# Kernel optimization log

Measured on AMD Instinct MI355X. Metric: run time of the kernel, lower is better.

## Reference

```python
import jax, jax.numpy as jnp
import numpy as np

D = 4096  # domain size of every variable X, Y, Z, W


def setup_inputs() -> dict:
    key = jax.random.key(0)
    ks = jax.random.split(key, 7)
    theta0 = jax.random.normal(ks[0], (D, D), dtype=jnp.float32)  # clique (X, Y)
    theta1 = jax.random.normal(ks[1], (D, D), dtype=jnp.float32)  # clique (Y, Z)
    theta2 = jax.random.normal(ks[2], (D, D), dtype=jnp.float32)  # clique (Z, W)
    ops = {f"op{i}": jax.random.randint(ks[3 + i], (2, D), 0, D, dtype=jnp.int32)
           for i in range(4)}
    return {"theta0": theta0, "theta1": theta1, "theta2": theta2, **ops}


def _remap(proc, op, dom):
    # torch: zeros(dom).index_add_(0, op[1], proc[op[0]])
    return jnp.zeros((dom,), proc.dtype).at[op[1]].add(proc[op[0]])


def reference(theta0, theta1, theta2, op0, op1, op2, op3):
    dom = theta0.shape[0]
    # m0: clique0 -> clique1 (forward): sum over X (dim 0), remap Y, broadcast over Z
    m0 = _remap(jnp.sum(theta0, axis=0), op0, dom)
    theta1 = theta1 + m0[:, None]          # reshape_dims [True, False]
    # m1: clique1 -> clique2 (forward): sum over Y (dim 0), remap Z
    m1 = _remap(jnp.sum(theta1, axis=0), op1, dom)
    theta2 = theta2 + m1[:, None]
    # m2: clique2 -> clique1 (backward): sum over W (dim 1), subtract stored fwd msg m1
    m2 = _remap(jnp.sum(theta2, axis=1) - m1, op2, dom)
    theta1 = theta1 + m2[None, :]          # reshape_dims [False, True]
    # m3: clique1 -> clique0 (backward): sum over Z (dim 1), subtract stored fwd msg m0
    m3 = _remap(jnp.sum(theta1, axis=1) - m0, op3, dom)
    theta0 = theta0 + m3[None, :]
    return (theta0, theta1, theta2)
```

## Files before the change

kernel.cpp:

```cpp
#include <hip/hip_runtime.h>

#define D 4096

typedef float fx4 __attribute__((ext_vector_type(4)));

#define CS0 0
#define CS1 D
#define RS1 (2 * D)
#define RS2 (3 * D)
#define M0O (4 * D)
#define M1O (5 * D)
#define M2O (6 * D)
#define M3O (7 * D)

__global__ void __launch_bounds__(256) reduce_kernel(
        const float* __restrict__ t0, const float* __restrict__ t1,
        float* __restrict__ ws) {
    int b = blockIdx.x;
    if (b < 512) {
        const float* A = (b < 256) ? t0 : t1;
        float* out = ws + ((b < 256) ? CS0 : CS1);
        int lb = b & 255;
        int c4 = (lb & 3) * 256 + threadIdx.x;
        int r0 = (lb >> 2) * 64;
        const fx4* A4 = (const fx4*)A;
        fx4 s = (fx4){0.f, 0.f, 0.f, 0.f};
        #pragma unroll 8
        for (int r = 0; r < 64; ++r)
            s += A4[(size_t)(r0 + r) * (D / 4) + c4];
        atomicAdd(&out[c4 * 4 + 0], s.x);
        atomicAdd(&out[c4 * 4 + 1], s.y);
        atomicAdd(&out[c4 * 4 + 2], s.z);
        atomicAdd(&out[c4 * 4 + 3], s.w);
    } else {
        int lb = b - 512;
        int wid = threadIdx.x >> 6, lane = threadIdx.x & 63;
        int row = lb * 4 + wid;
        const fx4* R = (const fx4*)(t1 + (size_t)row * D);
        float s = 0.f;
        #pragma unroll
        for (int j = 0; j < 16; ++j) {
            fx4 v = R[lane + 64 * j];
            s += (v.x + v.y) + (v.z + v.w);
        }
        #pragma unroll
        for (int o = 32; o > 0; o >>= 1) s += __shfl_down(s, o);
        if (lane == 0) ws[RS1 + row] = s;
    }
}


__device__ __forceinline__ float block_sum_1024(float v, float* red) {
    #pragma unroll
    for (int o = 32; o > 0; o >>= 1) v += __shfl_down(v, o);
    int lane = threadIdx.x & 63, wid = threadIdx.x >> 6;
    if (lane == 0) red[wid] = v;
    __syncthreads();
    if (threadIdx.x == 0) {
        float t = 0.f;
        #pragma unroll
        for (int w = 0; w < 16; ++w) t += red[w];
        red[0] = t;
    }
    __syncthreads();
    float r = red[0];
    __syncthreads();
    return r;
}

__global__ void __launch_bounds__(1024) msgsA_kernel(
        float* __restrict__ ws, const int* __restrict__ op0,
        const int* __restrict__ op1) {
    __shared__ float m0[D], m1[D];
    __shared__ float red[16];
    int tid = threadIdx.x;

    int s0[4], d0[4], s1[4], d1[4];
    #pragma unroll
    for (int k = 0; k < 4; ++k) {
        int i = tid + k * 1024;
        s0[k] = op0[i]; d0[k] = op0[D + i];
        s1[k] = op1[i]; d1[k] = op1[D + i];
    }
    float g0[4], g1[4];
    #pragma unroll
    for (int k = 0; k < 4; ++k) {
        g0[k] = ws[CS0 + s0[k]];
        g1[k] = ws[CS1 + s1[k]];
    }
    #pragma unroll
    for (int k = 0; k < 4; ++k) {
        int i = tid + k * 1024;
        m0[i] = 0.f; m1[i] = 0.f;
    }
    __syncthreads();
    #pragma unroll
    for (int k = 0; k < 4; ++k) atomicAdd(&m0[d0[k]], g0[k]);
    __syncthreads();
    float p = 0.f;
    #pragma unroll
    for (int k = 0; k < 4; ++k) p += m0[tid + k * 1024];
    float S0 = block_sum_1024(p, red);
    #pragma unroll
    for (int k = 0; k < 4; ++k) atomicAdd(&m1[d1[k]], g1[k] + S0);
    __syncthreads();
    #pragma unroll
    for (int k = 0; k < 4; ++k) {
        int i = tid + k * 1024;
        ws[M0O + i] = m0[i];
        ws[M1O + i] = m1[i];
    }
}

__global__ void __launch_bounds__(1024) msgsBC_kernel(
        float* __restrict__ ws, const int* __restrict__ op2,
        const int* __restrict__ op3) {
    __shared__ float m2[D], m3[D];
    __shared__ float red[16];
    int tid = threadIdx.x;

    int s2[4], d2[4], s3[4], d3[4];
    #pragma unroll
    for (int k = 0; k < 4; ++k) {
        int i = tid + k * 1024;
        s2[k] = op2[i]; d2[k] = op2[D + i];
        s3[k] = op3[i]; d3[k] = op3[D + i];
    }
    float g2[4], g3p[4];
    #pragma unroll
    for (int k = 0; k < 4; ++k) {
        g2[k]  = ws[RS2 + s2[k]] + 4095.0f * ws[M1O + s2[k]];
        g3p[k] = ws[RS1 + s3[k]] + 4095.0f * ws[M0O + s3[k]];
    }
    #pragma unroll
    for (int k = 0; k < 4; ++k) {
        int i = tid + k * 1024;
        m2[i] = 0.f; m3[i] = 0.f;
    }
    __syncthreads();
    #pragma unroll
    for (int k = 0; k < 4; ++k) atomicAdd(&m2[d2[k]], g2[k]);
    __syncthreads();
    float p = 0.f;
    #pragma unroll
    for (int k = 0; k < 4; ++k) p += m2[tid + k * 1024];
    float S2 = block_sum_1024(p, red);
    #pragma unroll
    for (int k = 0; k < 4; ++k) atomicAdd(&m3[d3[k]], g3p[k] + S2);
    __syncthreads();
    #pragma unroll
    for (int k = 0; k < 4; ++k) {
        int i = tid + k * 1024;
        ws[M2O + i] = m2[i];
        ws[M3O + i] = m3[i];
    }
}


__device__ __forceinline__ void row_reduce_store(float s, float* dst) {
    __shared__ float red[4];
    #pragma unroll
    for (int o = 32; o > 0; o >>= 1) s += __shfl_down(s, o);
    int lane = threadIdx.x & 63, wid = threadIdx.x >> 6;
    if (lane == 0) red[wid] = s;
    __syncthreads();
    if (threadIdx.x == 0) *dst = (red[0] + red[1]) + (red[2] + red[3]);
}

__global__ void __launch_bounds__(256) applyT2_kernel(
        const float* __restrict__ t2, float* __restrict__ ws,
        float* __restrict__ out2) {
    int row = blockIdx.x;
    size_t base = (size_t)row * D;
    const fx4* src = (const fx4*)(t2 + base);
    fx4* dst = (fx4*)(out2 + base);
    float rr = ws[M1O + row];

    fx4 v[4];
    float s = 0.f;
    #pragma unroll
    for (int k = 0; k < 4; ++k) {
        v[k] = src[threadIdx.x + 256 * k];
        s += (v[k].x + v[k].y) + (v[k].z + v[k].w);
    }
    #pragma unroll
    for (int k = 0; k < 4; ++k)
        __builtin_nontemporal_store(v[k] + rr, &dst[threadIdx.x + 256 * k]);
    row_reduce_store(s, ws + RS2 + row);
}

__global__ void __launch_bounds__(256) applyT1_kernel(
        const float* __restrict__ t1, const float* __restrict__ ws,
        float* __restrict__ out1) {
    int row = blockIdx.x;
    size_t base = (size_t)row * D;
    const fx4* src = (const fx4*)(t1 + base);
    const fx4* c4 = (const fx4*)(ws + M2O);
    fx4* dst = (fx4*)(out1 + base);
    float rr = ws[M0O + row];

    #pragma unroll
    for (int k = 0; k < 4; ++k) {
        fx4 r = src[threadIdx.x + 256 * k] + c4[threadIdx.x + 256 * k] + rr;
        __builtin_nontemporal_store(r, &dst[threadIdx.x + 256 * k]);
    }
}

__global__ void __launch_bounds__(256) applyT0_kernel(
        const float* __restrict__ t0, const float* __restrict__ ws,
        float* __restrict__ out0) {
    int row = blockIdx.x;
    size_t base = (size_t)row * D;
    const fx4* src = (const fx4*)(t0 + base);
    const fx4* c4 = (const fx4*)(ws + M3O);
    fx4* dst = (fx4*)(out0 + base);

    #pragma unroll
    for (int k = 0; k < 4; ++k) {
        fx4 r = src[threadIdx.x + 256 * k] + c4[threadIdx.x + 256 * k];
        __builtin_nontemporal_store(r, &dst[threadIdx.x + 256 * k]);
    }
}

extern "C" void kernel_launch(void* const* d_in, const int* in_sizes, int n_in,
                              void* d_out, int out_size, void* d_ws, size_t ws_size,
                              hipStream_t stream) {
    const float* t0 = (const float*)d_in[0];
    const float* t1 = (const float*)d_in[1];
    const float* t2 = (const float*)d_in[2];
    const int* op0 = (const int*)d_in[3];
    const int* op1 = (const int*)d_in[4];
    const int* op2 = (const int*)d_in[5];
    const int* op3 = (const int*)d_in[6];
    float* out = (float*)d_out;
    float* ws = (float*)d_ws;

    hipMemsetAsync(ws, 0, 2 * D * sizeof(float), stream);

    reduce_kernel<<<1536, 256, 0, stream>>>(t0, t1, ws);
    msgsA_kernel<<<1, 1024, 0, stream>>>(ws, op0, op1);
    applyT2_kernel<<<D, 256, 0, stream>>>(t2, ws, out + 2 * (size_t)D * D);
    msgsBC_kernel<<<1, 1024, 0, stream>>>(ws, op2, op3);
    applyT1_kernel<<<D, 256, 0, stream>>>(t1, ws, out + 1 * (size_t)D * D);
    applyT0_kernel<<<D, 256, 0, stream>>>(t0, ws, out + 0 * (size_t)D * D);
}
```

Before: 140.6 us.

## Fuse t1 row sums into column reduction pass and merge final apply kernels

The reduce kernel now computes t1's row sums in the same pass that accumulates its column sums, using per-row wave shuffles and a shared-memory partial array with atomics, instead of re-reading t1 in separate blocks. This removes one full 64MB read of t1. The t1 and t0 apply kernels are merged into a single launch of 2*D blocks, saving a launch and its tail. In exchange the t1 reduction blocks do a shuffle reduction per row, which adds ALU and shuffle work to a memory-bound loop, and the reduce grid drops to 512 blocks, which may leave the GPU under-occupied.

Measured after the change: 148.9 us. 1.06x slower.

```diff
diff --git a/kernel.cpp b/kernel.cpp
--- a/kernel.cpp
+++ b/kernel.cpp
@@ -16,36 +16,47 @@
 __global__ void __launch_bounds__(256) reduce_kernel(
         const float* __restrict__ t0, const float* __restrict__ t1,
         float* __restrict__ ws) {
-    int b = blockIdx.x;
-    if (b < 512) {
-        const float* A = (b < 256) ? t0 : t1;
-        float* out = ws + ((b < 256) ? CS0 : CS1);
-        int lb = b & 255;
-        int c4 = (lb & 3) * 256 + threadIdx.x;
-        int r0 = (lb >> 2) * 64;
-        const fx4* A4 = (const fx4*)A;
-        fx4 s = (fx4){0.f, 0.f, 0.f, 0.f};
+    int b = blockIdx.x, tid = threadIdx.x;
+    bool isT1 = (b >= 256);
+    const float* A = isT1 ? t1 : t0;
+    float* out = ws + (isT1 ? CS1 : CS0);
+    int lb = b & 255;
+    int c4 = (lb & 3) * 256 + tid;
+    int r0 = (lb >> 2) * 64;
+    const fx4* A4 = (const fx4*)A;
+    int lane = tid & 63, wv = tid >> 6;
+
+    __shared__ float rpart[64][4];
+    fx4 s = (fx4){0.f, 0.f, 0.f, 0.f};
+
+    if (isT1) {
+        #pragma unroll 4
+        for (int r = 0; r < 64; ++r) {
+            fx4 v = A4[(size_t)(r0 + r) * (D / 4) + c4];
+            s += v;
+            float rp = (v.x + v.y) + (v.z + v.w);
+            #pragma unroll
+            for (int o = 32; o > 0; o >>= 1) rp += __shfl_down(rp, o);
+            if (lane == 0) rpart[r][wv] = rp;
+        }
+    } else {
         #pragma unroll 8
         for (int r = 0; r < 64; ++r)
             s += A4[(size_t)(r0 + r) * (D / 4) + c4];
-        atomicAdd(&out[c4 * 4 + 0], s.x);
-        atomicAdd(&out[c4 * 4 + 1], s.y);
-        atomicAdd(&out[c4 * 4 + 2], s.z);
-        atomicAdd(&out[c4 * 4 + 3], s.w);
-    } else {
-        int lb = b - 512;
-        int wid = threadIdx.x >> 6, lane = threadIdx.x & 63;
-        int row = lb * 4 + wid;
-        const fx4* R = (const fx4*)(t1 + (size_t)row * D);
-        float s = 0.f;
-        #pragma unroll
-        for (int j = 0; j < 16; ++j) {
-            fx4 v = R[lane + 64 * j];
-            s += (v.x + v.y) + (v.z + v.w);
-        }
-        #pragma unroll
-        for (int o = 32; o > 0; o >>= 1) s += __shfl_down(s, o);
-        if (lane == 0) ws[RS1 + row] = s;
+    }
+
+    atomicAdd(&out[c4 * 4 + 0], s.x);
+    atomicAdd(&out[c4 * 4 + 1], s.y);
+    atomicAdd(&out[c4 * 4 + 2], s.z);
+    atomicAdd(&out[c4 * 4 + 3], s.w);
+
+    if (isT1) {
+        __syncthreads();
+        if (tid < 64) {
+            float rs = (rpart[tid][0] + rpart[tid][1]) +
+                       (rpart[tid][2] + rpart[tid][3]);
+            atomicAdd(&ws[RS1 + r0 + tid], rs);
+        }
     }
 }
 
@@ -154,17 +165,6 @@
         ws[M2O + i] = m2[i];
         ws[M3O + i] = m3[i];
     }
-}
-
-
-__device__ __forceinline__ void row_reduce_store(float s, float* dst) {
-    __shared__ float red[4];
-    #pragma unroll
-    for (int o = 32; o > 0; o >>= 1) s += __shfl_down(s, o);
-    int lane = threadIdx.x & 63, wid = threadIdx.x >> 6;
-    if (lane == 0) red[wid] = s;
-    __syncthreads();
-    if (threadIdx.x == 0) *dst = (red[0] + red[1]) + (red[2] + red[3]);
 }
 
 __global__ void __launch_bounds__(256) applyT2_kernel(
@@ -186,39 +186,43 @@
     #pragma unroll
     for (int k = 0; k < 4; ++k)
         __builtin_nontemporal_store(v[k] + rr, &dst[threadIdx.x + 256 * k]);
-    row_reduce_store(s, ws + RS2 + row);
-}
-
-__global__ void __launch_bounds__(256) applyT1_kernel(
-        const float* __restrict__ t1, const float* __restrict__ ws,
-        float* __restrict__ out1) {
-    int row = blockIdx.x;
+
+    __shared__ float red[4];
+    #pragma unroll
+    for (int o = 32; o > 0; o >>= 1) s += __shfl_down(s, o);
+    int lane = threadIdx.x & 63, wid = threadIdx.x >> 6;
+    if (lane == 0) red[wid] = s;
+    __syncthreads();
+    if (threadIdx.x == 0)
+        ws[RS2 + row] = (red[0] + red[1]) + (red[2] + red[3]);
+}
+
+__global__ void __launch_bounds__(256) applyT10_kernel(
+        const float* __restrict__ t0, const float* __restrict__ t1,
+        const float* __restrict__ ws, float* __restrict__ out) {
+    int b = blockIdx.x;
+    int row = b & (D - 1);
     size_t base = (size_t)row * D;
-    const fx4* src = (const fx4*)(t1 + base);
-    const fx4* c4 = (const fx4*)(ws + M2O);
-    fx4* dst = (fx4*)(out1 + base);
-    float rr = ws[M0O + row];
-
-    #pragma unroll
-    for (int k = 0; k < 4; ++k) {
-        fx4 r = src[threadIdx.x + 256 * k] + c4[threadIdx.x + 256 * k] + rr;
-        __builtin_nontemporal_store(r, &dst[threadIdx.x + 256 * k]);
-    }
-}
-
-__global__ void __launch_bounds__(256) applyT0_kernel(
-        const float* __restrict__ t0, const float* __restrict__ ws,
-        float* __restrict__ out0) {
-    int row = blockIdx.x;
-    size_t base = (size_t)row * D;
-    const fx4* src = (const fx4*)(t0 + base);
-    const fx4* c4 = (const fx4*)(ws + M3O);
-    fx4* dst = (fx4*)(out0 + base);
-
-    #pragma unroll
-    for (int k = 0; k < 4; ++k) {
-        fx4 r = src[threadIdx.x + 256 * k] + c4[threadIdx.x + 256 * k];
-        __builtin_nontemporal_store(r, &dst[threadIdx.x + 256 * k]);
+
+    if (b < D) {
+        const fx4* src = (const fx4*)(t1 + base);
+        const fx4* c4 = (const fx4*)(ws + M2O);
+        fx4* dst = (fx4*)(out + 1 * (size_t)D * D + base);
+        float rr = ws[M0O + row];
+        #pragma unroll
+        for (int k = 0; k < 4; ++k) {
+            fx4 r = src[threadIdx.x + 256 * k] + c4[threadIdx.x + 256 * k] + rr;
+            __builtin_nontemporal_store(r, &dst[threadIdx.x + 256 * k]);
+        }
+    } else {
+        const fx4* src = (const fx4*)(t0 + base);
+        const fx4* c4 = (const fx4*)(ws + M3O);
+        fx4* dst = (fx4*)(out + 0 * (size_t)D * D + base);
+        #pragma unroll
+        for (int k = 0; k < 4; ++k) {
+            fx4 r = src[threadIdx.x + 256 * k] + c4[threadIdx.x + 256 * k];
+            __builtin_nontemporal_store(r, &dst[threadIdx.x + 256 * k]);
+        }
     }
 }
 
@@ -235,12 +239,11 @@
     float* out = (float*)d_out;
     float* ws = (float*)d_ws;
 
-    hipMemsetAsync(ws, 0, 2 * D * sizeof(float), stream);
-
-    reduce_kernel<<<1536, 256, 0, stream>>>(t0, t1, ws);
+    hipMemsetAsync(ws, 0, 3 * D * sizeof(float), stream);
+
+    reduce_kernel<<<512, 256, 0, stream>>>(t0, t1, ws);
     msgsA_kernel<<<1, 1024, 0, stream>>>(ws, op0, op1);
     applyT2_kernel<<<D, 256, 0, stream>>>(t2, ws, out + 2 * (size_t)D * D);
     msgsBC_kernel<<<1, 1024, 0, stream>>>(ws, op2, op3);
-    applyT1_kernel<<<D, 256, 0, stream>>>(t1, ws, out + 1 * (size_t)D * D);
-    applyT0_kernel<<<D, 256, 0, stream>>>(t0, ws, out + 0 * (size_t)D * D);
-}
+    applyT10_kernel<<<2 * D, 256, 0, stream>>>(t0, t1, ws, out);
+}
```
